# Performance work log

Hardware: AMD Instinct MI355X
Metric: run time of the kernel (lower is better)

The kernel has to match this reference:

```python
import jax, jax.numpy as jnp
import numpy as np

B, T, N, SD, D, HYP, EMB = 128, 256, 8, 200, 64, 64, 32

def _ln(x, g, b, eps=1e-5):
    mu = jnp.mean(x, -1, keepdims=True)
    v = jnp.mean((x - mu) ** 2, -1, keepdims=True)
    return (x - mu) * jax.lax.rsqrt(v + eps) * g + b

def setup_inputs():
    key = jax.random.key(0)
    ks = iter(jax.random.split(key, 64))
    def p(shape, scale=0.05):
        return (jax.random.normal(next(ks), shape) * scale).astype(jnp.float32)
    n, sd, d, hyp, emb = N, SD, D, HYP, EMB
    return dict(
        qvals=p((B, T, n), 1.0), states=p((B, T, sd), 1.0), hidden_state=p((B, T, n, d), 1.0),
        enc_w1=p((sd, d)), enc_b1=p((d,)), enc_w2=p((d, d)), enc_b2=p((d,)),
        wq=p((d, d)), bq=p((d,)), wk=p((d, d)), bk=p((d,)), wv=p((d, d)), bv=p((d,)),
        wo=p((d, d)), bo=p((d,)),
        ln1_g=jnp.ones((d,), jnp.float32), ln1_b=jnp.zeros((d,), jnp.float32),
        ffn_w1=p((d, d)), ffn_b1=p((d,)), ffn_w2=p((d, d)), ffn_b2=p((d,)),
        ln2_g=jnp.ones((d,), jnp.float32), ln2_b=jnp.zeros((d,), jnp.float32),
        fc2ni_w=p((n, d, n - 1)), fc2ni_b=p((n, n - 1)),
        norm_g=jnp.ones((n - 1,), jnp.float32), norm_b=jnp.zeros((n - 1,), jnp.float32),
        w1a=p((2 * d, hyp)), b1a=p((hyp,)), w1b=p((hyp, n * emb)), b1b=p((n * emb,)),
        hb1w=p((2 * d, emb)), hb1b=p((emb,)),
        w2a=p((2 * d, hyp)), b2a=p((hyp,)), w2b=p((hyp, emb)), b2b=p((emb,)),
        hb2w1=p((2 * d, emb)), hb2b1=p((emb,)), hb2w2=p((emb, 1)), hb2b2=p((1,)))

def reference(qvals, states, hidden_state, enc_w1, enc_b1, enc_w2, enc_b2,
              wq, bq, wk, bk, wv, bv, wo, bo, ln1_g, ln1_b,
              ffn_w1, ffn_b1, ffn_w2, ffn_b2, ln2_g, ln2_b,
              fc2ni_w, fc2ni_b, norm_g, norm_b,
              w1a, b1a, w1b, b1b, hb1w, hb1b,
              w2a, b2a, w2b, b2b, hb2w1, hb2b1, hb2w2, hb2b2):
    sg = jax.lax.stop_gradient
    b, t, n = qvals.shape
    bt = b * t
    d = hidden_state.shape[-1]
    emb = hb1w.shape[1]
    # Encoder_s: relu(fc1) then tanh(fc2(e)+e)
    s = states.reshape(bt, -1)
    e = jax.nn.relu(s @ enc_w1 + enc_b1)
    enc = jnp.tanh(e @ enc_w2 + enc_b2 + e)                       # (bt, 64)
    # concat detached agent hiddens with detached state embedding -> (bt, n+1, 64)
    h = jnp.concatenate([sg(hidden_state.reshape(bt, n, d)), sg(enc)[:, None, :]], axis=1)
    # transformer block (single-head self-attention + FFN, post-LN)
    q = h @ wq + bq; k = h @ wk + bk; v = h @ wv + bv
    att = jax.nn.softmax(jnp.einsum('bid,bjd->bij', q, k) / jnp.sqrt(jnp.float32(d)), axis=-1)
    h2 = _ln(h + (att @ v) @ wo + bo, ln1_g, ln1_b)
    h3 = _ln(h2 + jax.nn.relu(h2 @ ffn_w1 + ffn_b1) @ ffn_w2 + ffn_b2, ln2_g, ln2_b)
    h_trans = h3[:, :n]                                           # (bt, n, 64)
    ens = jnp.concatenate([enc, sg(h_trans).mean(1)], axis=-1)    # (bt, 128)
    # per-agent fc2_Ni -> LayerNorm -> sigmoid, vectorized over agents
    ni = jnp.einsum('xnd,nde->xne', h_trans, fc2ni_w) + fc2ni_b   # (bt, n, n-1)
    ni = jax.nn.sigmoid(_ln(ni, norm_g, norm_b))
    # insert 1.0 at the diagonal (agent i keeps its own q with weight 1)
    rows = jnp.arange(n)[:, None]; cols = jnp.arange(n)[None, :]
    gidx = jnp.clip(cols - (cols > rows).astype(jnp.int32), 0, n - 2)  # (n, n)
    gathered = jnp.take_along_axis(ni, jnp.broadcast_to(gidx, (bt, n, n)), axis=-1)
    nfull = jnp.where(cols == rows, jnp.float32(1.0), gathered)   # (bt, n, n)
    N_nn = nfull.reshape(b, t, n, n)
    q_ni = (qvals[:, :, None, :] * N_nn).sum(-1).reshape(bt, 1, n)
    # hypernetwork mixing (QMIX)
    ens_d = sg(ens)
    w1 = jnp.abs(jax.nn.relu(ens_d @ w1a + b1a) @ w1b + b1b).reshape(bt, n, emb)
    b1 = (ens_d @ hb1w + hb1b).reshape(bt, 1, emb)
    w2 = jnp.abs(jax.nn.relu(ens @ w2a + b2a) @ w2b + b2b).reshape(bt, emb, 1)
    b2 = (jax.nn.relu(ens @ hb2w1 + hb2b1) @ hb2w2 + hb2b2).reshape(bt, 1, 1)
    hidden = jax.nn.elu(q_ni @ w1 + b1)
    y = (hidden @ w2 + b2).reshape(b, t, 1)
    eye_mask = jnp.broadcast_to(jnp.eye(n, dtype=bool), (b, t, n, n))
    return y, N_nn, eye_mask
```

## Files before the change

### kernel.cpp

```cpp
#include <hip/hip_runtime.h>
#include <hip/hip_bf16.h>

typedef __bf16 bf16x8 __attribute__((ext_vector_type(8)));
typedef __bf16 bf16x4 __attribute__((ext_vector_type(4)));
typedef float f32x4 __attribute__((ext_vector_type(4)));

#define ROWSG 32768
#define RB 8
#define HPAD 72
#define NN_OFF ((size_t)ROWSG)
#define EYE_OFF ((size_t)ROWSG + (size_t)ROWSG*64)

#define OFF_EW1   0
#define OFF_EW2   14336
#define OFF_WQ    18432
#define OFF_WK    22528
#define OFF_WV    26624
#define OFF_WO    30720
#define OFF_F1    34816
#define OFF_F2    38912
#define OFF_W1A   43008
#define OFF_W1B   51200
#define OFF_HB1W  67584
#define OFF_W2A   71680
#define OFF_W2B   79872
#define OFF_HB2W1 81920
#define WS_TOTAL  86016

__device__ __align__(16) __bf16 g_ws[WS_TOTAL];

#define MFMA16(a,b,c) __builtin_amdgcn_mfma_f32_16x16x32_bf16(a,b,c,0,0,0)

struct TP { const float* src[14]; };

__global__ __launch_bounds__(256) void wtrans(TP tp) {
    const int gid = blockIdx.x * 256 + threadIdx.x;
    if (gid >= WS_TOTAL) return;
    const int OFFS[14] = {OFF_EW1, OFF_EW2, OFF_WQ, OFF_WK, OFF_WV, OFF_WO, OFF_F1,
                          OFF_F2, OFF_W1A, OFF_W1B, OFF_HB1W, OFF_W2A, OFF_W2B, OFF_HB2W1};
    const int KPS[14]  = {224, 64, 64, 64, 64, 64, 64, 64, 128, 64, 128, 128, 64, 128};
    const int KRS[14]  = {200, 64, 64, 64, 64, 64, 64, 64, 128, 64, 128, 128, 64, 128};
    const int NS[14]   = {64, 64, 64, 64, 64, 64, 64, 64, 64, 256, 32, 64, 32, 32};
    int m = 0;
#pragma unroll
    for (int i = 1; i < 14; ++i) if (gid >= OFFS[i]) m = i;
    const int loc = gid - OFFS[m];
    const int Kp = KPS[m];
    const int n = loc / Kp;
    const int k = loc - n * Kp;
    float v = 0.f;
    if (k < KRS[m]) v = tp.src[m][(size_t)k * NS[m] + n];
    g_ws[gid] = (__bf16)v;
}

struct MainP {
    const float *qvals, *states, *hid, *eb1, *eb2, *bq, *bk, *bv, *bo,
        *l1g, *l1b, *fb1, *fb2, *l2g, *l2b, *niw, *nib, *ng, *nb,
        *b1a, *b1b, *hb1b, *b2a, *b2b, *hb2b1, *hw2, *hb2b2;
    float* out;
};

__device__ __forceinline__ void proj_ln(const __bf16* A, const __bf16* WT,
                                        const float* bias, const float* g, const float* bb,
                                        __bf16* H, int w, int quad, int l15) {
    for (int mti = 0; mti < 2; ++mti) {
        const int mt = w + 4 * mti;
        if (mt >= 5) continue;
        f32x4 acc0 = {0,0,0,0}, acc1 = {0,0,0,0}, acc2 = {0,0,0,0}, acc3 = {0,0,0,0};
#pragma unroll
        for (int ks = 0; ks < 2; ++ks) {
            const int kk = ks * 32 + quad * 8;
            const bf16x8 af = *(const bf16x8*)(A + (mt * 16 + l15) * HPAD + kk);
            acc0 = MFMA16(af, *(const bf16x8*)(WT + (size_t)(0 * 16 + l15) * 64 + kk), acc0);
            acc1 = MFMA16(af, *(const bf16x8*)(WT + (size_t)(1 * 16 + l15) * 64 + kk), acc1);
            acc2 = MFMA16(af, *(const bf16x8*)(WT + (size_t)(2 * 16 + l15) * 64 + kk), acc2);
            acc3 = MFMA16(af, *(const bf16x8*)(WT + (size_t)(3 * 16 + l15) * 64 + kk), acc3);
        }
        float v[4][4], g4[4], b4[4];
#pragma unroll
        for (int nt = 0; nt < 4; ++nt) {
            const int col = nt * 16 + l15;
            const float bo = bias[col];
            g4[nt] = g[col]; b4[nt] = bb[col];
            const f32x4 a = (nt == 0) ? acc0 : (nt == 1) ? acc1 : (nt == 2) ? acc2 : acc3;
#pragma unroll
            for (int r = 0; r < 4; ++r)
                v[nt][r] = a[r] + bo + (float)H[(mt * 16 + quad * 4 + r) * HPAD + col];
        }
#pragma unroll
        for (int r = 0; r < 4; ++r) {
            float s  = v[0][r] + v[1][r] + v[2][r] + v[3][r];
            float s2 = v[0][r]*v[0][r] + v[1][r]*v[1][r] + v[2][r]*v[2][r] + v[3][r]*v[3][r];
#pragma unroll
            for (int off = 1; off < 16; off <<= 1) {
                s  += __shfl_xor(s,  off, 64);
                s2 += __shfl_xor(s2, off, 64);
            }
            const float mu  = s * 0.015625f;
            const float var = s2 * 0.015625f - mu * mu;
            const float rs  = rsqrtf(var + 1e-5f);
#pragma unroll
            for (int nt = 0; nt < 4; ++nt)
                H[(mt * 16 + quad * 4 + r) * HPAD + nt * 16 + l15] =
                    (__bf16)((v[nt][r] - mu) * rs * g4[nt] + b4[nt]);
        }
    }
}

__global__ __launch_bounds__(256) void mixer_main(MainP p) {
    __shared__ __align__(16) __bf16 Hb[80 * HPAD];
    __shared__ __align__(16) __bf16 QbU[80 * HPAD];
    __shared__ __align__(16) __bf16 KbU[80 * HPAD];
    __shared__ __align__(16) __bf16 EbU[16 * HPAD];
    __shared__ float  attU[8 * 81];
    __shared__ float  sQv[64];
    __shared__ float  qniL[64];

    __bf16* Sb   = QbU;
    __bf16* Qb   = QbU;
    __bf16* Kb   = KbU;
    __bf16* W1bS = QbU;
    float*  B1f  = (float*)(QbU + 2048);
    float*  W2f  = (float*)(QbU + 2560);
    float*  T3f  = (float*)(QbU + 3072);
    __bf16* Tb2  = QbU + 3584;
    __bf16* ensB = KbU;

    const int blk = blockIdx.x;
    const int bt0 = blk * RB;
    const int t = threadIdx.x;
    const int w = t >> 6, lane = t & 63, quad = lane >> 4, l15 = lane & 15;
    const __bf16* ws = g_ws;

#pragma unroll
    for (int it = 0; it < 4; ++it) {
        const int u = it * 256 + t;
        const int x = u >> 7, rem = u & 127, n = rem >> 4, d4 = (rem & 15) * 4;
        const float4 v4 = *(const float4*)(p.hid + ((size_t)(bt0 + x) * 512 + n * 64 + d4));
        bf16x4 o; o[0] = (__bf16)v4.x; o[1] = (__bf16)v4.y; o[2] = (__bf16)v4.z; o[3] = (__bf16)v4.w;
        *(bf16x4*)(Hb + (x * 9 + n) * HPAD + d4) = o;
    }
#pragma unroll
    for (int it = 0; it < 2; ++it) {
        const int u = it * 256 + t;
        if (u < 400) {
            const int xr = u / 50, c4 = u - xr * 50;
            const float4 v4 = *(const float4*)(p.states + (size_t)(bt0 + xr) * 200 + c4 * 4);
            bf16x4 o; o[0] = (__bf16)v4.x; o[1] = (__bf16)v4.y; o[2] = (__bf16)v4.z; o[3] = (__bf16)v4.w;
            *(bf16x4*)(Sb + xr * 224 + c4 * 4) = o;
        }
    }
    if (t < 192) { const int xr = t / 24, c = t - xr * 24; Sb[xr * 224 + 200 + c] = (__bf16)0.0f; }
    if (t < 64) sQv[t] = p.qvals[(size_t)(bt0 + (t >> 3)) * 8 + (t & 7)];
    __syncthreads();

    float e4[4];
    {
        const int n0 = w * 16;
        const int srow = (l15 < 8) ? l15 : 7;
        f32x4 acc = {0, 0, 0, 0};
        for (int ks = 0; ks < 7; ++ks) {
            const int kk = ks * 32 + quad * 8;
            const bf16x8 af = *(const bf16x8*)(Sb + srow * 224 + kk);
            const bf16x8 bf = *(const bf16x8*)(ws + OFF_EW1 + (size_t)(n0 + l15) * 224 + kk);
            acc = MFMA16(af, bf, acc);
        }
        const float b1 = p.eb1[n0 + l15];
#pragma unroll
        for (int r = 0; r < 4; ++r) {
            const float ev = fmaxf(acc[r] + b1, 0.f);
            e4[r] = ev;
            EbU[(quad * 4 + r) * HPAD + n0 + l15] = (__bf16)ev;
        }
    }
    __syncthreads();

    {
        const int n0 = w * 16;
        f32x4 acc = {0, 0, 0, 0};
#pragma unroll
        for (int ks = 0; ks < 2; ++ks) {
            const int kk = ks * 32 + quad * 8;
            const bf16x8 af = *(const bf16x8*)(EbU + l15 * HPAD + kk);
            const bf16x8 bf = *(const bf16x8*)(ws + OFF_EW2 + (size_t)(n0 + l15) * 64 + kk);
            acc = MFMA16(af, bf, acc);
        }
        const float b2 = p.eb2[n0 + l15];
#pragma unroll
        for (int r = 0; r < 4; ++r) {
            const int xr = quad * 4 + r;
            if (xr < RB) {
                const float ev = tanhf(acc[r] + e4[r] + b2);
                Hb[(xr * 9 + 8) * HPAD + n0 + l15] = (__bf16)ev;
                EbU[(8 + xr) * HPAD + n0 + l15] = (__bf16)ev;
            }
        }
    }
    __syncthreads();

    for (int it = 0; it < 10; ++it) {
        const int j = w + 4 * it;
        const int mat = j / 20, r20 = j % 20, mt = r20 >> 2, nt = r20 & 3;
        const __bf16* wt = ws + (mat == 0 ? OFF_WQ : OFF_WK);
        const float* bias = (mat == 0 ? p.bq : p.bk);
        __bf16* dst = (mat == 0 ? Qb : Kb);
        f32x4 acc = {0, 0, 0, 0};
#pragma unroll
        for (int ks = 0; ks < 2; ++ks) {
            const int kk = ks * 32 + quad * 8;
            const bf16x8 af = *(const bf16x8*)(Hb + (mt * 16 + l15) * HPAD + kk);
            const bf16x8 bf = *(const bf16x8*)(wt + (size_t)(nt * 16 + l15) * 64 + kk);
            acc = MFMA16(af, bf, acc);
        }
        const float bv = bias[nt * 16 + l15];
#pragma unroll
        for (int r = 0; r < 4; ++r)
            dst[(mt * 16 + quad * 4 + r) * HPAD + nt * 16 + l15] = (__bf16)(acc[r] + bv);
    }
    __syncthreads();

    for (int xi = 0; xi < 2; ++xi) {
        const int x = w * 2 + xi;
        const int arow = (x * 9 + l15) * HPAD;
        f32x4 acc = {0, 0, 0, 0};
#pragma unroll
        for (int ks = 0; ks < 2; ++ks) {
            const int kk = ks * 32 + quad * 8;
            const bf16x8 qa = *(const bf16x8*)(Qb + arow + kk);
            const bf16x8 kb = *(const bf16x8*)(Kb + arow + kk);
            acc = MFMA16(qa, kb, acc);
        }
#pragma unroll
        for (int r = 0; r < 4; ++r) {
            const int i = quad * 4 + r;
            float s = (l15 < 9) ? acc[r] * 0.125f : -3.0e38f;
            float m = s;
#pragma unroll
            for (int off = 1; off < 16; off <<= 1) m = fmaxf(m, __shfl_xor(m, off, 64));
            float e = (l15 < 9) ? __expf(s - m) : 0.f;
            float sum = e;
#pragma unroll
            for (int off = 1; off < 16; off <<= 1) sum += __shfl_xor(sum, off, 64);
            const float pv = e / sum;
            if (i < 9 && l15 < 9) attU[x * 81 + i * 9 + l15] = pv;
        }
    }
    __syncthreads();

    for (int xi = 0; xi < 2; ++xi) {
        const int x = w * 2 + xi;
        float vreg[9];
#pragma unroll
        for (int jj = 0; jj < 9; ++jj) vreg[jj] = (float)Hb[(x * 9 + jj) * HPAD + lane];
#pragma unroll
        for (int i = 0; i < 9; ++i) {
            float a = 0.f;
#pragma unroll
            for (int jj = 0; jj < 9; ++jj) a += attU[x * 81 + i * 9 + jj] * vreg[jj];
            Kb[(x * 9 + i) * HPAD + lane] = (__bf16)a;
        }
    }
    __syncthreads();

    for (int it = 0; it < 5; ++it) {
        const int j = w + 4 * it;
        const int mt = j >> 2, nt = j & 3;
        f32x4 acc = {0, 0, 0, 0};
#pragma unroll
        for (int ks = 0; ks < 2; ++ks) {
            const int kk = ks * 32 + quad * 8;
            const bf16x8 af = *(const bf16x8*)(Kb + (mt * 16 + l15) * HPAD + kk);
            const bf16x8 bf = *(const bf16x8*)(ws + OFF_WV + (size_t)(nt * 16 + l15) * 64 + kk);
            acc = MFMA16(af, bf, acc);
        }
        const float bv = p.bv[nt * 16 + l15];
#pragma unroll
        for (int r = 0; r < 4; ++r)
            Qb[(mt * 16 + quad * 4 + r) * HPAD + nt * 16 + l15] = (__bf16)(acc[r] + bv);
    }
    __syncthreads();

    proj_ln(Qb, ws + OFF_WO, p.bo, p.l1g, p.l1b, Hb, w, quad, l15);
    __syncthreads();

    for (int it = 0; it < 5; ++it) {
        const int j = w + 4 * it;
        const int mt = j >> 2, nt = j & 3;
        f32x4 acc = {0, 0, 0, 0};
#pragma unroll
        for (int ks = 0; ks < 2; ++ks) {
            const int kk = ks * 32 + quad * 8;
            const bf16x8 af = *(const bf16x8*)(Hb + (mt * 16 + l15) * HPAD + kk);
            const bf16x8 bf = *(const bf16x8*)(ws + OFF_F1 + (size_t)(nt * 16 + l15) * 64 + kk);
            acc = MFMA16(af, bf, acc);
        }
        const float fb = p.fb1[nt * 16 + l15];
#pragma unroll
        for (int r = 0; r < 4; ++r)
            Kb[(mt * 16 + quad * 4 + r) * HPAD + nt * 16 + l15] = (__bf16)fmaxf(acc[r] + fb, 0.f);
    }
    __syncthreads();

    proj_ln(Kb, ws + OFF_F2, p.fb2, p.l2g, p.l2b, Hb, w, quad, l15);
    __syncthreads();

#pragma unroll
    for (int it = 0; it < 2; ++it) {
        const int id = it * 256 + t;
        const int x = id >> 6, col = id & 63;
        float s = 0.f;
#pragma unroll
        for (int i = 0; i < 8; ++i) s += (float)Hb[(x * 9 + i) * HPAD + col];
        ensB[x * 136 + 64 + col] = (__bf16)(s * 0.125f);
        ensB[x * 136 + col] = EbU[(8 + x) * HPAD + col];
    }
    __syncthreads();

    {
        const int pr = t >> 2, q4 = t & 3;
        const int x = pr >> 3, n = pr & 7;
        float acc[7] = {0.f, 0.f, 0.f, 0.f, 0.f, 0.f, 0.f};
        const float* wni = p.niw + n * 448;
        for (int dd = 0; dd < 16; ++dd) {
            const int d = q4 * 16 + dd;
            const float hv = (float)Hb[(x * 9 + n) * HPAD + d];
#pragma unroll
            for (int e = 0; e < 7; ++e) acc[e] += hv * wni[d * 7 + e];
        }
#pragma unroll
        for (int e = 0; e < 7; ++e) {
            acc[e] += __shfl_xor(acc[e], 1, 64);
            acc[e] += __shfl_xor(acc[e], 2, 64);
        }
        if (q4 == 0) {
            float s = 0.f;
#pragma unroll
            for (int e = 0; e < 7; ++e) { acc[e] += p.nib[n * 7 + e]; s += acc[e]; }
            const float mu = s * (1.f / 7.f);
            float s2 = 0.f;
#pragma unroll
            for (int e = 0; e < 7; ++e) { const float d0 = acc[e] - mu; s2 += d0 * d0; }
            const float rs = rsqrtf(s2 * (1.f / 7.f) + 1e-5f);
            float* sNi = (float*)EbU;
#pragma unroll
            for (int e = 0; e < 7; ++e) {
                const float vv = (acc[e] - mu) * rs * p.ng[e] + p.nb[e];
                sNi[x * 64 + n * 8 + e] = 1.f / (1.f + __expf(-vv));
            }
        }
    }
    __syncthreads();

    {
        const float* sNi = (const float*)EbU;
        float* Nf = attU;
#pragma unroll
        for (int it = 0; it < 2; ++it) {
            const int id = it * 256 + t;
            const int x = id >> 6, rem = id & 63, i = rem >> 3, jj = rem & 7;
            const float nf = (i == jj) ? 1.f : sNi[x * 64 + i * 8 + (jj - (jj > i ? 1 : 0))];
            p.out[NN_OFF + (size_t)(bt0 + x) * 64 + rem] = nf;
            p.out[EYE_OFF + (size_t)(bt0 + x) * 64 + rem] = (i == jj) ? 1.f : 0.f;
            Nf[x * 64 + rem] = nf;
        }
    }
    __syncthreads();

    {
        const float* Nf = attU;
        const int pr = t >> 2, q4 = t & 3;
        const int x = pr >> 3, i = pr & 7;
        const int j0 = q4 * 2;
        float s = sQv[x * 8 + j0] * Nf[x * 64 + i * 8 + j0] +
                  sQv[x * 8 + j0 + 1] * Nf[x * 64 + i * 8 + j0 + 1];
        s += __shfl_xor(s, 1, 64);
        s += __shfl_xor(s, 2, 64);
        if (q4 == 0) qniL[x * 8 + i] = s;
    }
    {
        const int n0 = w * 16;
#pragma unroll
        for (int m2 = 0; m2 < 2; ++m2) {
            const __bf16* wt = ws + (m2 == 0 ? OFF_W1A : OFF_W2A);
            const float* bias = m2 == 0 ? p.b1a : p.b2a;
            __bf16* dst = m2 == 0 ? EbU : Tb2;
            f32x4 acc = {0, 0, 0, 0};
#pragma unroll
            for (int ks = 0; ks < 4; ++ks) {
                const int kk = ks * 32 + quad * 8;
                const bf16x8 af = *(const bf16x8*)(ensB + l15 * 136 + kk);
                const bf16x8 bf = *(const bf16x8*)(wt + (size_t)(n0 + l15) * 128 + kk);
                acc = MFMA16(af, bf, acc);
            }
            const float bb = bias[n0 + l15];
#pragma unroll
            for (int r = 0; r < 4; ++r)
                dst[(quad * 4 + r) * HPAD + n0 + l15] = (__bf16)fmaxf(acc[r] + bb, 0.f);
        }
    }
    __syncthreads();

    for (int it = 0; it < 6; ++it) {
        const int j = w + 4 * it;
        if (j >= 22) continue;
        int mode, n0, Kp, ksteps, aStride;
        const __bf16 *A, *WT; const float* bias;
        if (j < 16)      { mode = 0; n0 = j * 16;        A = EbU;  aStride = HPAD; WT = ws + OFF_W1B;   bias = p.b1b;  Kp = 64;  ksteps = 2; }
        else if (j < 18) { mode = 1; n0 = (j - 16) * 16; A = ensB; aStride = 136;  WT = ws + OFF_HB1W;  bias = p.hb1b; Kp = 128; ksteps = 4; }
        else if (j < 20) { mode = 2; n0 = (j - 18) * 16; A = Tb2;  aStride = HPAD; WT = ws + OFF_W2B;   bias = p.b2b;  Kp = 64;  ksteps = 2; }
        else             { mode = 3; n0 = (j - 20) * 16; A = ensB; aStride = 136;  WT = ws + OFF_HB2W1; bias = p.hb2b1;Kp = 128; ksteps = 4; }
        f32x4 acc = {0, 0, 0, 0};
        for (int ks = 0; ks < ksteps; ++ks) {
            const int kk = ks * 32 + quad * 8;
            const bf16x8 af = *(const bf16x8*)(A + l15 * aStride + kk);
            const bf16x8 bf = *(const bf16x8*)(WT + (size_t)(n0 + l15) * Kp + kk);
            acc = MFMA16(af, bf, acc);
        }
        const float bb = bias[n0 + l15];
#pragma unroll
        for (int r = 0; r < 4; ++r) {
            const int xr = quad * 4 + r;
            if (xr < RB) {
                const float val = acc[r] + bb;
                if (mode == 0)      W1bS[xr * 256 + n0 + l15] = (__bf16)fabsf(val);
                else if (mode == 1) B1f[xr * 32 + n0 + l15] = val;
                else if (mode == 2) W2f[xr * 32 + n0 + l15] = fabsf(val);
                else                T3f[xr * 32 + n0 + l15] = fmaxf(val, 0.f);
            }
        }
    }
    __syncthreads();

    if (t < 128) {
        const int x = t >> 4, sub = t & 15;
        float pp = 0.f, pb = 0.f;
#pragma unroll
        for (int h2i = 0; h2i < 2; ++h2i) {
            const int e = sub + h2i * 16;
            float a = B1f[x * 32 + e];
#pragma unroll
            for (int i = 0; i < 8; ++i) a += qniL[x * 8 + i] * (float)W1bS[x * 256 + i * 32 + e];
            const float hid = a > 0.f ? a : (__expf(a) - 1.f);
            pp += hid * W2f[x * 32 + e];
            pb += T3f[x * 32 + e] * p.hw2[e];
        }
#pragma unroll
        for (int off = 1; off < 16; off <<= 1) {
            pp += __shfl_xor(pp, off, 64);
            pb += __shfl_xor(pb, off, 64);
        }
        if (sub == 0) p.out[bt0 + x] = pp + pb + p.hb2b2[0];
    }
}

extern "C" void kernel_launch(void* const* d_in, const int* in_sizes, int n_in,
                              void* d_out, int out_size, void* d_ws, size_t ws_size,
                              hipStream_t stream) {
    TP tp;
    tp.src[0]  = (const float*)d_in[3];
    tp.src[1]  = (const float*)d_in[5];
    tp.src[2]  = (const float*)d_in[7];
    tp.src[3]  = (const float*)d_in[9];
    tp.src[4]  = (const float*)d_in[11];
    tp.src[5]  = (const float*)d_in[13];
    tp.src[6]  = (const float*)d_in[17];
    tp.src[7]  = (const float*)d_in[19];
    tp.src[8]  = (const float*)d_in[27];
    tp.src[9]  = (const float*)d_in[29];
    tp.src[10] = (const float*)d_in[31];
    tp.src[11] = (const float*)d_in[33];
    tp.src[12] = (const float*)d_in[35];
    tp.src[13] = (const float*)d_in[37];
    wtrans<<<(WS_TOTAL + 255) / 256, 256, 0, stream>>>(tp);

    MainP p;
    p.qvals = (const float*)d_in[0];
    p.states = (const float*)d_in[1];
    p.hid = (const float*)d_in[2];
    p.eb1 = (const float*)d_in[4];
    p.eb2 = (const float*)d_in[6];
    p.bq = (const float*)d_in[8];
    p.bk = (const float*)d_in[10];
    p.bv = (const float*)d_in[12];
    p.bo = (const float*)d_in[14];
    p.l1g = (const float*)d_in[15];
    p.l1b = (const float*)d_in[16];
    p.fb1 = (const float*)d_in[18];
    p.fb2 = (const float*)d_in[20];
    p.l2g = (const float*)d_in[21];
    p.l2b = (const float*)d_in[22];
    p.niw = (const float*)d_in[23];
    p.nib = (const float*)d_in[24];
    p.ng = (const float*)d_in[25];
    p.nb = (const float*)d_in[26];
    p.b1a = (const float*)d_in[28];
    p.b1b = (const float*)d_in[30];
    p.hb1b = (const float*)d_in[32];
    p.b2a = (const float*)d_in[34];
    p.b2b = (const float*)d_in[36];
    p.hb2b1 = (const float*)d_in[38];
    p.hw2 = (const float*)d_in[39];
    p.hb2b2 = (const float*)d_in[40];
    p.out = (float*)d_out;

    mixer_main<<<ROWSG / RB, 256, 0, stream>>>(p);
}
```

Baseline: 402.5 us.

## Use 6 rows per block to fit 64-row MFMA tiles; MFMA for agent-interaction head

Lowers rows per block from 8 to 6, so the 54 token rows (6×9) fit in four 16-row MFMA tiles instead of five. This removes the uneven fifth tile and shrinks shared memory, with bounds clamping for the partial last block. The per-agent fc2ni projection moves from scalar FMAs reading fp32 weights from global memory to MFMA over a pre-transposed bf16 weight block in the workspace. The two attention stages are merged into one loop, dropping one barrier. Risks: more blocks, each carrying the same fixed weight-load overhead, and padded lanes wasted in MFMA.

```diff
diff --git a/kernel.cpp b/kernel.cpp
--- a/kernel.cpp
+++ b/kernel.cpp
@@ -6,7 +6,8 @@
 typedef float f32x4 __attribute__((ext_vector_type(4)));
 
 #define ROWSG 32768
-#define RB 8
+#define RB 6
+#define NBLK 5462
 #define HPAD 72
 #define NN_OFF ((size_t)ROWSG)
 #define EYE_OFF ((size_t)ROWSG + (size_t)ROWSG*64)
@@ -25,17 +26,25 @@
 #define OFF_W2A   71680
 #define OFF_W2B   79872
 #define OFF_HB2W1 81920
-#define WS_TOTAL  86016
+#define OFF_NI    86016
+#define WS_TOTAL  94208
 
 __device__ __align__(16) __bf16 g_ws[WS_TOTAL];
 
 #define MFMA16(a,b,c) __builtin_amdgcn_mfma_f32_16x16x32_bf16(a,b,c,0,0,0)
 
-struct TP { const float* src[14]; };
+struct TP { const float* src[15]; };
 
 __global__ __launch_bounds__(256) void wtrans(TP tp) {
     const int gid = blockIdx.x * 256 + threadIdx.x;
     if (gid >= WS_TOTAL) return;
+    if (gid >= OFF_NI) {
+        const int loc = gid - OFF_NI;
+        const int nmat = loc >> 10, rem = loc & 1023, e = rem >> 6, k = rem & 63;
+        float v = (e < 7) ? tp.src[14][nmat * 448 + k * 7 + e] : 0.f;
+        g_ws[gid] = (__bf16)v;
+        return;
+    }
     const int OFFS[14] = {OFF_EW1, OFF_EW2, OFF_WQ, OFF_WK, OFF_WV, OFF_WO, OFF_F1,
                           OFF_F2, OFF_W1A, OFF_W1B, OFF_HB1W, OFF_W2A, OFF_W2B, OFF_HB2W1};
     const int KPS[14]  = {224, 64, 64, 64, 64, 64, 64, 64, 128, 64, 128, 128, 64, 128};
@@ -60,71 +69,67 @@
     float* out;
 };
 
-__device__ __forceinline__ void proj_ln(const __bf16* A, const __bf16* WT,
-                                        const float* bias, const float* g, const float* bb,
-                                        __bf16* H, int w, int quad, int l15) {
-    for (int mti = 0; mti < 2; ++mti) {
-        const int mt = w + 4 * mti;
-        if (mt >= 5) continue;
-        f32x4 acc0 = {0,0,0,0}, acc1 = {0,0,0,0}, acc2 = {0,0,0,0}, acc3 = {0,0,0,0};
-#pragma unroll
-        for (int ks = 0; ks < 2; ++ks) {
-            const int kk = ks * 32 + quad * 8;
-            const bf16x8 af = *(const bf16x8*)(A + (mt * 16 + l15) * HPAD + kk);
-            acc0 = MFMA16(af, *(const bf16x8*)(WT + (size_t)(0 * 16 + l15) * 64 + kk), acc0);
-            acc1 = MFMA16(af, *(const bf16x8*)(WT + (size_t)(1 * 16 + l15) * 64 + kk), acc1);
-            acc2 = MFMA16(af, *(const bf16x8*)(WT + (size_t)(2 * 16 + l15) * 64 + kk), acc2);
-            acc3 = MFMA16(af, *(const bf16x8*)(WT + (size_t)(3 * 16 + l15) * 64 + kk), acc3);
-        }
-        float v[4][4], g4[4], b4[4];
-#pragma unroll
-        for (int nt = 0; nt < 4; ++nt) {
-            const int col = nt * 16 + l15;
-            const float bo = bias[col];
-            g4[nt] = g[col]; b4[nt] = bb[col];
-            const f32x4 a = (nt == 0) ? acc0 : (nt == 1) ? acc1 : (nt == 2) ? acc2 : acc3;
-#pragma unroll
-            for (int r = 0; r < 4; ++r)
-                v[nt][r] = a[r] + bo + (float)H[(mt * 16 + quad * 4 + r) * HPAD + col];
-        }
-#pragma unroll
-        for (int r = 0; r < 4; ++r) {
-            float s  = v[0][r] + v[1][r] + v[2][r] + v[3][r];
-            float s2 = v[0][r]*v[0][r] + v[1][r]*v[1][r] + v[2][r]*v[2][r] + v[3][r]*v[3][r];
-#pragma unroll
-            for (int off = 1; off < 16; off <<= 1) {
-                s  += __shfl_xor(s,  off, 64);
-                s2 += __shfl_xor(s2, off, 64);
-            }
-            const float mu  = s * 0.015625f;
-            const float var = s2 * 0.015625f - mu * mu;
-            const float rs  = rsqrtf(var + 1e-5f);
-#pragma unroll
-            for (int nt = 0; nt < 4; ++nt)
-                H[(mt * 16 + quad * 4 + r) * HPAD + nt * 16 + l15] =
-                    (__bf16)((v[nt][r] - mu) * rs * g4[nt] + b4[nt]);
-        }
+__device__ __forceinline__ void proj_ln4(const __bf16* A, const __bf16* WT,
+                                         const float* bias, const float* g, const float* bb,
+                                         __bf16* H, int w, int quad, int l15) {
+    const int mt = w;
+    f32x4 acc0 = {0,0,0,0}, acc1 = {0,0,0,0}, acc2 = {0,0,0,0}, acc3 = {0,0,0,0};
+#pragma unroll
+    for (int ks = 0; ks < 2; ++ks) {
+        const int kk = ks * 32 + quad * 8;
+        const bf16x8 af = *(const bf16x8*)(A + (mt * 16 + l15) * HPAD + kk);
+        acc0 = MFMA16(af, *(const bf16x8*)(WT + (size_t)(0 * 16 + l15) * 64 + kk), acc0);
+        acc1 = MFMA16(af, *(const bf16x8*)(WT + (size_t)(1 * 16 + l15) * 64 + kk), acc1);
+        acc2 = MFMA16(af, *(const bf16x8*)(WT + (size_t)(2 * 16 + l15) * 64 + kk), acc2);
+        acc3 = MFMA16(af, *(const bf16x8*)(WT + (size_t)(3 * 16 + l15) * 64 + kk), acc3);
+    }
+    float v[4][4], g4[4], b4[4];
+#pragma unroll
+    for (int nt = 0; nt < 4; ++nt) {
+        const int col = nt * 16 + l15;
+        const float bo = bias[col];
+        g4[nt] = g[col]; b4[nt] = bb[col];
+        const f32x4 a = (nt == 0) ? acc0 : (nt == 1) ? acc1 : (nt == 2) ? acc2 : acc3;
+#pragma unroll
+        for (int r = 0; r < 4; ++r)
+            v[nt][r] = a[r] + bo + (float)H[(mt * 16 + quad * 4 + r) * HPAD + col];
+    }
+#pragma unroll
+    for (int r = 0; r < 4; ++r) {
+        float s  = v[0][r] + v[1][r] + v[2][r] + v[3][r];
+        float s2 = v[0][r]*v[0][r] + v[1][r]*v[1][r] + v[2][r]*v[2][r] + v[3][r]*v[3][r];
+#pragma unroll
+        for (int off = 1; off < 16; off <<= 1) {
+            s  += __shfl_xor(s,  off, 64);
+            s2 += __shfl_xor(s2, off, 64);
+        }
+        const float mu  = s * 0.015625f;
+        const float var = s2 * 0.015625f - mu * mu;
+        const float rs  = rsqrtf(var + 1e-5f);
+#pragma unroll
+        for (int nt = 0; nt < 4; ++nt)
+            H[(mt * 16 + quad * 4 + r) * HPAD + nt * 16 + l15] =
+                (__bf16)((v[nt][r] - mu) * rs * g4[nt] + b4[nt]);
     }
 }
 
 __global__ __launch_bounds__(256) void mixer_main(MainP p) {
-    __shared__ __align__(16) __bf16 Hb[80 * HPAD];
-    __shared__ __align__(16) __bf16 QbU[80 * HPAD];
-    __shared__ __align__(16) __bf16 KbU[80 * HPAD];
+    __shared__ __align__(16) __bf16 Hb[64 * HPAD];
+    __shared__ __align__(16) __bf16 Qb[64 * HPAD];
+    __shared__ __align__(16) __bf16 Kb[64 * HPAD];
     __shared__ __align__(16) __bf16 EbU[16 * HPAD];
-    __shared__ float  attU[8 * 81];
-    __shared__ float  sQv[64];
-    __shared__ float  qniL[64];
-
-    __bf16* Sb   = QbU;
-    __bf16* Qb   = QbU;
-    __bf16* Kb   = KbU;
-    __bf16* W1bS = QbU;
-    float*  B1f  = (float*)(QbU + 2048);
-    float*  W2f  = (float*)(QbU + 2560);
-    float*  T3f  = (float*)(QbU + 3072);
-    __bf16* Tb2  = QbU + 3584;
-    __bf16* ensB = KbU;
+    __shared__ float  attU[6 * 81];
+    __shared__ float  sQv[48];
+    __shared__ float  qniL[48];
+
+    __bf16* Sb   = Qb;
+    __bf16* W1bS = Qb;
+    float*  B1f  = (float*)(Qb + 1536);
+    float*  W2f  = (float*)(Qb + 1920);
+    float*  T3f  = (float*)(Qb + 2304);
+    __bf16* Tb2  = Qb + 2688;
+    float*  sNiP = (float*)(Qb + 3840);
+    __bf16* ensB = Kb;
 
     const int blk = blockIdx.x;
     const int bt0 = blk * RB;
@@ -133,31 +138,39 @@
     const __bf16* ws = g_ws;
 
 #pragma unroll
-    for (int it = 0; it < 4; ++it) {
+    for (int it = 0; it < 3; ++it) {
         const int u = it * 256 + t;
         const int x = u >> 7, rem = u & 127, n = rem >> 4, d4 = (rem & 15) * 4;
-        const float4 v4 = *(const float4*)(p.hid + ((size_t)(bt0 + x) * 512 + n * 64 + d4));
+        const int bt = bt0 + x;
+        const size_t btc = (bt < ROWSG) ? bt : (ROWSG - 1);
+        const float4 v4 = *(const float4*)(p.hid + (btc * 512 + n * 64 + d4));
         bf16x4 o; o[0] = (__bf16)v4.x; o[1] = (__bf16)v4.y; o[2] = (__bf16)v4.z; o[3] = (__bf16)v4.w;
         *(bf16x4*)(Hb + (x * 9 + n) * HPAD + d4) = o;
     }
 #pragma unroll
     for (int it = 0; it < 2; ++it) {
         const int u = it * 256 + t;
-        if (u < 400) {
+        if (u < 300) {
             const int xr = u / 50, c4 = u - xr * 50;
-            const float4 v4 = *(const float4*)(p.states + (size_t)(bt0 + xr) * 200 + c4 * 4);
+            const int bt = bt0 + xr;
+            const size_t btc = (bt < ROWSG) ? bt : (ROWSG - 1);
+            const float4 v4 = *(const float4*)(p.states + btc * 200 + c4 * 4);
             bf16x4 o; o[0] = (__bf16)v4.x; o[1] = (__bf16)v4.y; o[2] = (__bf16)v4.z; o[3] = (__bf16)v4.w;
             *(bf16x4*)(Sb + xr * 224 + c4 * 4) = o;
         }
     }
-    if (t < 192) { const int xr = t / 24, c = t - xr * 24; Sb[xr * 224 + 200 + c] = (__bf16)0.0f; }
-    if (t < 64) sQv[t] = p.qvals[(size_t)(bt0 + (t >> 3)) * 8 + (t & 7)];
+    if (t < 144) { const int xr = t / 24, c = t - xr * 24; Sb[xr * 224 + 200 + c] = (__bf16)0.0f; }
+    if (t < 48) {
+        const int bt = bt0 + (t >> 3);
+        const size_t btc = (bt < ROWSG) ? bt : (ROWSG - 1);
+        sQv[t] = p.qvals[btc * 8 + (t & 7)];
+    }
     __syncthreads();
 
     float e4[4];
     {
         const int n0 = w * 16;
-        const int srow = (l15 < 8) ? l15 : 7;
+        const int srow = (l15 < RB) ? l15 : (RB - 1);
         f32x4 acc = {0, 0, 0, 0};
         for (int ks = 0; ks < 7; ++ks) {
             const int kk = ks * 32 + quad * 8;
@@ -198,9 +211,9 @@
     }
     __syncthreads();
 
-    for (int it = 0; it < 10; ++it) {
+    for (int it = 0; it < 8; ++it) {
         const int j = w + 4 * it;
-        const int mat = j / 20, r20 = j % 20, mt = r20 >> 2, nt = r20 & 3;
+        const int mat = j >> 4, r16 = j & 15, mt = r16 >> 2, nt = r16 & 3;
         const __bf16* wt = ws + (mat == 0 ? OFF_WQ : OFF_WK);
         const float* bias = (mat == 0 ? p.bq : p.bk);
         __bf16* dst = (mat == 0 ? Qb : Kb);
@@ -221,48 +234,48 @@
 
     for (int xi = 0; xi < 2; ++xi) {
         const int x = w * 2 + xi;
-        const int arow = (x * 9 + l15) * HPAD;
-        f32x4 acc = {0, 0, 0, 0};
-#pragma unroll
-        for (int ks = 0; ks < 2; ++ks) {
-            const int kk = ks * 32 + quad * 8;
-            const bf16x8 qa = *(const bf16x8*)(Qb + arow + kk);
-            const bf16x8 kb = *(const bf16x8*)(Kb + arow + kk);
-            acc = MFMA16(qa, kb, acc);
-        }
-#pragma unroll
-        for (int r = 0; r < 4; ++r) {
-            const int i = quad * 4 + r;
-            float s = (l15 < 9) ? acc[r] * 0.125f : -3.0e38f;
-            float m = s;
-#pragma unroll
-            for (int off = 1; off < 16; off <<= 1) m = fmaxf(m, __shfl_xor(m, off, 64));
-            float e = (l15 < 9) ? __expf(s - m) : 0.f;
-            float sum = e;
-#pragma unroll
-            for (int off = 1; off < 16; off <<= 1) sum += __shfl_xor(sum, off, 64);
-            const float pv = e / sum;
-            if (i < 9 && l15 < 9) attU[x * 81 + i * 9 + l15] = pv;
-        }
-    }
-    __syncthreads();
-
-    for (int xi = 0; xi < 2; ++xi) {
-        const int x = w * 2 + xi;
-        float vreg[9];
-#pragma unroll
-        for (int jj = 0; jj < 9; ++jj) vreg[jj] = (float)Hb[(x * 9 + jj) * HPAD + lane];
-#pragma unroll
-        for (int i = 0; i < 9; ++i) {
-            float a = 0.f;
-#pragma unroll
-            for (int jj = 0; jj < 9; ++jj) a += attU[x * 81 + i * 9 + jj] * vreg[jj];
-            Kb[(x * 9 + i) * HPAD + lane] = (__bf16)a;
-        }
-    }
-    __syncthreads();
-
-    for (int it = 0; it < 5; ++it) {
+        if (x >= RB) continue;
+        {
+            const int arow = (x * 9 + l15) * HPAD;
+            f32x4 acc = {0, 0, 0, 0};
+#pragma unroll
+            for (int ks = 0; ks < 2; ++ks) {
+                const int kk = ks * 32 + quad * 8;
+                const bf16x8 qa = *(const bf16x8*)(Qb + arow + kk);
+                const bf16x8 kb = *(const bf16x8*)(Kb + arow + kk);
+                acc = MFMA16(qa, kb, acc);
+            }
+#pragma unroll
+            for (int r = 0; r < 4; ++r) {
+                const int i = quad * 4 + r;
+                float s = (l15 < 9) ? acc[r] * 0.125f : -3.0e38f;
+                float m = s;
+#pragma unroll
+                for (int off = 1; off < 16; off <<= 1) m = fmaxf(m, __shfl_xor(m, off, 64));
+                float e = (l15 < 9) ? __expf(s - m) : 0.f;
+                float sum = e;
+#pragma unroll
+                for (int off = 1; off < 16; off <<= 1) sum += __shfl_xor(sum, off, 64);
+                const float pv = e / sum;
+                if (i < 9 && l15 < 9) attU[x * 81 + i * 9 + l15] = pv;
+            }
+        }
+        {
+            float vreg[9];
+#pragma unroll
+            for (int jj = 0; jj < 9; ++jj) vreg[jj] = (float)Hb[(x * 9 + jj) * HPAD + lane];
+#pragma unroll
+            for (int i = 0; i < 9; ++i) {
+                float a = 0.f;
+#pragma unroll
+                for (int jj = 0; jj < 9; ++jj) a += attU[x * 81 + i * 9 + jj] * vreg[jj];
+                Kb[(x * 9 + i) * HPAD + lane] = (__bf16)a;
+            }
+        }
+    }
+    __syncthreads();
+
+    for (int it = 0; it < 4; ++it) {
         const int j = w + 4 * it;
         const int mt = j >> 2, nt = j & 3;
         f32x4 acc = {0, 0, 0, 0};
@@ -280,10 +293,10 @@
     }
     __syncthreads();
 
-    proj_ln(Qb, ws + OFF_WO, p.bo, p.l1g, p.l1b, Hb, w, quad, l15);
-    __syncthreads();
-
-    for (int it = 0; it < 5; ++it) {
+    proj_ln4(Qb, ws + OFF_WO, p.bo, p.l1g, p.l1b, Hb, w, quad, l15);
+    __syncthreads();
+
+    for (int it = 0; it < 4; ++it) {
         const int j = w + 4 * it;
         const int mt = j >> 2, nt = j & 3;
         f32x4 acc = {0, 0, 0, 0};
@@ -301,72 +314,76 @@
     }
     __syncthreads();
 
-    proj_ln(Kb, ws + OFF_F2, p.fb2, p.l2g, p.l2b, Hb, w, quad, l15);
-    __syncthreads();
-
-#pragma unroll
-    for (int it = 0; it < 2; ++it) {
-        const int id = it * 256 + t;
-        const int x = id >> 6, col = id & 63;
-        float s = 0.f;
-#pragma unroll
-        for (int i = 0; i < 8; ++i) s += (float)Hb[(x * 9 + i) * HPAD + col];
-        ensB[x * 136 + 64 + col] = (__bf16)(s * 0.125f);
-        ensB[x * 136 + col] = EbU[(8 + x) * HPAD + col];
-    }
+    proj_ln4(Kb, ws + OFF_F2, p.fb2, p.l2g, p.l2b, Hb, w, quad, l15);
     __syncthreads();
 
     {
-        const int pr = t >> 2, q4 = t & 3;
-        const int x = pr >> 3, n = pr & 7;
-        float acc[7] = {0.f, 0.f, 0.f, 0.f, 0.f, 0.f, 0.f};
-        const float* wni = p.niw + n * 448;
-        for (int dd = 0; dd < 16; ++dd) {
-            const int d = q4 * 16 + dd;
-            const float hv = (float)Hb[(x * 9 + n) * HPAD + d];
-#pragma unroll
-            for (int e = 0; e < 7; ++e) acc[e] += hv * wni[d * 7 + e];
-        }
-#pragma unroll
-        for (int e = 0; e < 7; ++e) {
-            acc[e] += __shfl_xor(acc[e], 1, 64);
-            acc[e] += __shfl_xor(acc[e], 2, 64);
-        }
-        if (q4 == 0) {
-            float s = 0.f;
-#pragma unroll
-            for (int e = 0; e < 7; ++e) { acc[e] += p.nib[n * 7 + e]; s += acc[e]; }
-            const float mu = s * (1.f / 7.f);
-            float s2 = 0.f;
-#pragma unroll
-            for (int e = 0; e < 7; ++e) { const float d0 = acc[e] - mu; s2 += d0 * d0; }
+        const int id = t;
+#pragma unroll
+        for (int it = 0; it < 2; ++it) {
+            const int u = it * 256 + id;
+            if (u < 384) {
+                const int x = u >> 6, col = u & 63;
+                float s = 0.f;
+#pragma unroll
+                for (int i = 0; i < 8; ++i) s += (float)Hb[(x * 9 + i) * HPAD + col];
+                ensB[x * 136 + 64 + col] = (__bf16)(s * 0.125f);
+                ensB[x * 136 + col] = EbU[(8 + x) * HPAD + col];
+            }
+        }
+    }
+    for (int jn = 0; jn < 2; ++jn) {
+        const int n = w * 2 + jn;
+        const int l15c = (l15 < RB) ? l15 : (RB - 1);
+        f32x4 acc = {0, 0, 0, 0};
+#pragma unroll
+        for (int ks = 0; ks < 2; ++ks) {
+            const int kk = ks * 32 + quad * 8;
+            const bf16x8 af = *(const bf16x8*)(Hb + (l15c * 9 + n) * HPAD + kk);
+            const bf16x8 bf = *(const bf16x8*)(ws + OFF_NI + n * 1024 + (size_t)l15 * 64 + kk);
+            acc = MFMA16(af, bf, acc);
+        }
+#pragma unroll
+        for (int r = 0; r < 4; ++r) {
+            const int x = quad * 4 + r;
+            const float av = (l15 < 7) ? (acc[r] + p.nib[n * 7 + l15]) : 0.f;
+            float s1 = av;
+            s1 += __shfl_xor(s1, 1, 64); s1 += __shfl_xor(s1, 2, 64);
+            s1 += __shfl_xor(s1, 4, 64); s1 += __shfl_xor(s1, 8, 64);
+            const float mu = s1 * (1.f / 7.f);
+            float d0 = (l15 < 7) ? (av - mu) : 0.f;
+            float s2 = d0 * d0;
+            s2 += __shfl_xor(s2, 1, 64); s2 += __shfl_xor(s2, 2, 64);
+            s2 += __shfl_xor(s2, 4, 64); s2 += __shfl_xor(s2, 8, 64);
             const float rs = rsqrtf(s2 * (1.f / 7.f) + 1e-5f);
-            float* sNi = (float*)EbU;
-#pragma unroll
-            for (int e = 0; e < 7; ++e) {
-                const float vv = (acc[e] - mu) * rs * p.ng[e] + p.nb[e];
-                sNi[x * 64 + n * 8 + e] = 1.f / (1.f + __expf(-vv));
+            if (x < RB && l15 < 7) {
+                const float vv = (av - mu) * rs * p.ng[l15] + p.nb[l15];
+                sNiP[(x * 8 + n) * 7 + l15] = 1.f / (1.f + __expf(-vv));
             }
         }
     }
     __syncthreads();
 
     {
-        const float* sNi = (const float*)EbU;
         float* Nf = attU;
 #pragma unroll
         for (int it = 0; it < 2; ++it) {
-            const int id = it * 256 + t;
-            const int x = id >> 6, rem = id & 63, i = rem >> 3, jj = rem & 7;
-            const float nf = (i == jj) ? 1.f : sNi[x * 64 + i * 8 + (jj - (jj > i ? 1 : 0))];
-            p.out[NN_OFF + (size_t)(bt0 + x) * 64 + rem] = nf;
-            p.out[EYE_OFF + (size_t)(bt0 + x) * 64 + rem] = (i == jj) ? 1.f : 0.f;
-            Nf[x * 64 + rem] = nf;
-        }
-    }
-    __syncthreads();
-
-    {
+            const int u = it * 256 + t;
+            if (u < 384) {
+                const int x = u >> 6, rem = u & 63, i = rem >> 3, jj = rem & 7;
+                const float nf = (i == jj) ? 1.f : sNiP[(x * 8 + i) * 7 + jj - (jj > i ? 1 : 0)];
+                const int bt = bt0 + x;
+                if (bt < ROWSG) {
+                    p.out[NN_OFF + (size_t)bt * 64 + rem] = nf;
+                    p.out[EYE_OFF + (size_t)bt * 64 + rem] = (i == jj) ? 1.f : 0.f;
+                }
+                Nf[x * 64 + rem] = nf;
+            }
+        }
+    }
+    __syncthreads();
+
+    if (t < 192) {
         const float* Nf = attU;
         const int pr = t >> 2, q4 = t & 3;
         const int x = pr >> 3, i = pr & 7;
@@ -431,7 +448,7 @@
     }
     __syncthreads();
 
-    if (t < 128) {
+    if (t < 96) {
         const int x = t >> 4, sub = t & 15;
         float pp = 0.f, pb = 0.f;
 #pragma unroll
@@ -449,7 +466,8 @@
             pp += __shfl_xor(pp, off, 64);
             pb += __shfl_xor(pb, off, 64);
         }
-        if (sub == 0) p.out[bt0 + x] = pp + pb + p.hb2b2[0];
+        const int bt = bt0 + x;
+        if (sub == 0 && bt < ROWSG) p.out[bt] = pp + pb + p.hb2b2[0];
     }
 }
 
@@ -471,6 +489,7 @@
     tp.src[11] = (const float*)d_in[33];
     tp.src[12] = (const float*)d_in[35];
     tp.src[13] = (const float*)d_in[37];
+    tp.src[14] = (const float*)d_in[23];
     wtrans<<<(WS_TOTAL + 255) / 256, 256, 0, stream>>>(tp);
 
     MainP p;
@@ -503,5 +522,5 @@
     p.hb2b2 = (const float*)d_in[40];
     p.out = (float*)d_out;
 
-    mixer_main<<<ROWSG / RB, 256, 0, stream>>>(p);
+    mixer_main<<<NBLK, 256, 0, stream>>>(p);
 }
```

Result: no change. 397.6 us (-1.2%).
